# Kernel tuning notes

Measured on AMD Instinct MI355X. Metric: run time of the kernel, lower is better.

## Reference

```python
import jax, jax.numpy as jnp
import numpy as np

A_, H_, D_, T_, B_ = 12, 6, 192, 80, 8
C_ = 192                      # GATv2 out_channels per head
N_ = B_ * A_                  # sequences
G_ = B_ * T_                  # graphs (one per frame)
E_ = A_ * (A_ - 1)            # 132 directed edges, no self loops
DH_ = D_ // H_


def _ln(x, g, b):
    m = jnp.mean(x, -1, keepdims=True)
    v = jnp.mean((x - m) ** 2, -1, keepdims=True)
    return (x - m) * jax.lax.rsqrt(v + 1e-5) * g + b


def _bn(x, g, b, m, v):  # eval-mode BatchNorm1d over the feature channel
    return (x - m) * jax.lax.rsqrt(v + 1e-5) * g + b


def _forward(state_feat, edge_attr, emb_table, laW1, lab1, bn1g, bn1b, bn1m, bn1v, laW2, lab2, bn2g, bn2b, bn2m, bn2v, laW3, lab3, bn3g, bn3b, bn3m, bn3v, ln1g, ln1b, qkvw, qkvb, outw, outb, ln2g, ln2b, fw1, fb1, fw2, fb2, gwl, gbl, gwr, gbr, gwe, gatt, gbias, ng, nb, padding_mask, agent_ids, edge_index):
    pl = emb_table[jnp.clip(agent_ids, 0)]                                   # [N,12]
    x = jnp.concatenate([state_feat, jnp.broadcast_to(pl[:, None, :], (N_, T_, 12))], -1)
    x = jax.nn.relu(_bn(x @ laW1 + lab1, bn1g, bn1b, bn1m, bn1v))
    x = jax.nn.relu(_bn(x @ laW2 + lab2, bn2g, bn2b, bn2m, bn2v))
    x = jax.nn.relu(_bn(x @ laW3 + lab3, bn3g, bn3b, bn3m, bn3v))
    x_initial = x
    # sinusoidal positional encoding (dropout off / eval)
    pos = jnp.arange(T_, dtype=jnp.float32)[:, None]
    div = jnp.exp(jnp.arange(0, D_, 2, dtype=jnp.float32) * (-np.log(10000.0) / D_))
    pe = jnp.zeros((T_, D_), jnp.float32).at[:, 0::2].set(jnp.sin(pos * div)).at[:, 1::2].set(jnp.cos(pos * div))
    x = x + pe
    causal = jnp.triu(jnp.full((T_, T_), -jnp.inf, jnp.float32), k=1)
    # --- static GAT edge structure (shared by every frame-graph) ---
    src, dst = edge_index[0], edge_index[1]
    onehot = (dst[None, :] == jnp.arange(A_)[:, None]).astype(jnp.float32)   # [A,E]
    cnt = onehot.sum(1)
    ea = edge_attr.reshape(G_, E_, 2)
    # PyG add_self_loops(fill_value='mean'): self-loop attr = mean of incoming-edge attrs
    loop_ea = jnp.einsum('ae,gef->gaf', onehot, ea) / cnt[None, :, None]     # [G,A,2]
    ea2 = jnp.concatenate([ea, loop_ea], axis=1).reshape(-1, 2)              # [G*(E+A),2]
    src2 = jnp.concatenate([src, jnp.arange(A_, dtype=src.dtype)])
    dst2 = jnp.concatenate([dst, jnp.arange(A_, dtype=dst.dtype)])
    off = (jnp.arange(G_, dtype=src.dtype) * A_)[:, None]
    sflat = (src2[None, :] + off).reshape(-1)                                # flattened batch-of-graphs
    dflat = (dst2[None, :] + off).reshape(-1)
    GA = G_ * A_
    for l in range(3):
        # --- causal temporal self-attention (pre-LN, eval: dropout off) ---
        xn = _ln(x, ln1g[l], ln1b[l])
        qkv = xn @ qkvw[l] + qkvb[l]
        q, k, v = jnp.split(qkv, 3, axis=-1)
        q = q.reshape(N_, T_, H_, DH_); k = k.reshape(N_, T_, H_, DH_); v = v.reshape(N_, T_, H_, DH_)
        s = jnp.einsum('nqhd,nkhd->nhqk', q, k) / np.sqrt(DH_) + causal
        s = jnp.where(padding_mask[:, None, None, :], -jnp.inf, s)
        p = jax.nn.softmax(s, axis=-1)
        o = jnp.einsum('nhqk,nkhd->nqhd', p, v).reshape(N_, T_, D_)
        x = x + (o @ outw[l] + outb[l])
        xn = _ln(x, ln2g[l], ln2b[l])
        x = x + (jax.nn.gelu(xn @ fw1[l] + fb1[l], approximate=False) @ fw2[l] + fb2[l])
        # --- framewise GATv2 (concat=False -> mean over heads) ---
        xn = _ln(x, ng[l], nb[l])
        xnodes = xn.reshape(B_, A_, T_, D_).transpose(0, 2, 1, 3).reshape(GA, D_)
        xl = (xnodes @ gwl[l] + gbl[l]).reshape(GA, H_, C_)
        xr = (xnodes @ gwr[l] + gbr[l]).reshape(GA, H_, C_)
        ef = (ea2 @ gwe[l]).reshape(-1, H_, C_)
        xls = xl[sflat]                                                      # gather source features
        msg = jax.nn.leaky_relu(xls + xr[dflat] + ef, 0.2)
        alpha = jnp.einsum('ehc,hc->eh', msg, gatt[l])
        amax = jax.lax.stop_gradient(jax.ops.segment_max(alpha, dflat, num_segments=GA))
        exs = jnp.exp(alpha - amax[dflat])
        den = jax.ops.segment_sum(exs, dflat, num_segments=GA)
        w = exs / den[dflat]                                                 # segment softmax over dst
        agg = jax.ops.segment_sum(w[:, :, None] * xls, dflat, num_segments=GA)
        xg = (agg.mean(axis=1) + gbias[l]).reshape(B_, T_, A_, D_).transpose(0, 2, 1, 3).reshape(N_, T_, D_)
        x = x + xg
    return (x_initial, x)


def setup_inputs():
    ks = iter(jax.random.split(jax.random.key(0), 60))
    def r(shape, s=0.05):
        return jax.random.normal(next(ks), shape, jnp.float32) * s
    pairs = np.array([(i, j) for i in range(A_) for j in range(A_) if i != j], dtype=np.int32)
    return dict(
        state_feat=jax.random.normal(next(ks), (N_, T_, 4), jnp.float32),
        padding_mask=jnp.zeros((N_, T_), bool),
        agent_ids=jax.random.randint(next(ks), (N_,), 0, 600, jnp.int32),
        edge_index=jnp.asarray(pairs.T),
        edge_attr=jax.random.normal(next(ks), (B_, T_, E_, 2), jnp.float32),
        emb_table=r((600, 12), 1.0),
        laW1=r((16, 64)), lab1=jnp.zeros((64,)),
        bn1g=jnp.ones((64,)), bn1b=jnp.zeros((64,)), bn1m=jnp.zeros((64,)), bn1v=jnp.ones((64,)),
        laW2=r((64, 256)), lab2=jnp.zeros((256,)),
        bn2g=jnp.ones((256,)), bn2b=jnp.zeros((256,)), bn2m=jnp.zeros((256,)), bn2v=jnp.ones((256,)),
        laW3=r((256, D_)), lab3=jnp.zeros((D_,)),
        bn3g=jnp.ones((D_,)), bn3b=jnp.zeros((D_,)), bn3m=jnp.zeros((D_,)), bn3v=jnp.ones((D_,)),
        ln1g=jnp.ones((3, D_)), ln1b=jnp.zeros((3, D_)),
        qkvw=r((3, D_, 3 * D_)), qkvb=jnp.zeros((3, 3 * D_)),
        outw=r((3, D_, D_)), outb=jnp.zeros((3, D_)),
        ln2g=jnp.ones((3, D_)), ln2b=jnp.zeros((3, D_)),
        fw1=r((3, D_, 4 * D_)), fb1=jnp.zeros((3, 4 * D_)),
        fw2=r((3, 4 * D_, D_)), fb2=jnp.zeros((3, D_)),
        gwl=r((3, D_, H_ * C_)), gbl=jnp.zeros((3, H_ * C_)),
        gwr=r((3, D_, H_ * C_)), gbr=jnp.zeros((3, H_ * C_)),
        gwe=r((3, 2, H_ * C_)),
        gatt=r((3, H_, C_)),
        gbias=jnp.zeros((3, D_)),
        ng=jnp.ones((3, D_)), nb=jnp.zeros((3, D_)),
    )


def reference(state_feat, padding_mask, agent_ids, edge_index, edge_attr, emb_table, laW1, lab1, bn1g, bn1b, bn1m, bn1v, laW2, lab2, bn2g, bn2b, bn2m, bn2v, laW3, lab3, bn3g, bn3b, bn3m, bn3v, ln1g, ln1b, qkvw, qkvb, outw, outb, ln2g, ln2b, fw1, fb1, fw2, fb2, gwl, gbl, gwr, gbr, gwe, gatt, gbias, ng, nb):
    return _forward(state_feat, edge_attr, emb_table, laW1, lab1, bn1g, bn1b, bn1m, bn1v, laW2, lab2, bn2g, bn2b, bn2m, bn2v, laW3, lab3, bn3g, bn3b, bn3m, bn3v, ln1g, ln1b, qkvw, qkvb, outw, outb, ln2g, ln2b, fw1, fb1, fw2, fb2, gwl, gbl, gwr, gbr, gwe, gatt, gbias, ng, nb, padding_mask, agent_ids, edge_index)
```

## Files before the change

### kernel.cpp

```cpp
#include <hip/hip_runtime.h>
#include <hip/hip_bf16.h>
#include <math.h>

#define A_   12
#define H_   6
#define N_   96
#define T_   80
#define G_   640
#define E_   132
#define E2_  144
#define ROWS_ 7680

typedef const __hip_bfloat16* bfp;
typedef __hip_bfloat16 bf16;
typedef __attribute__((ext_vector_type(8))) short short8;
typedef __attribute__((ext_vector_type(4))) short short4v;
typedef __attribute__((ext_vector_type(4))) float f32x4;
typedef _Float16 h2 __attribute__((ext_vector_type(2)));

#define WB_QKV   0
#define WB_OUT   331776
#define WB_FW1   442368
#define WB_FW2   884736
#define WB_GAT   1327104
#define WB_W1    2654208
#define WB_W2    2655232
#define WB_W3T   2671616
#define WB_GWE   2720768
#define WB_GATT  2727680
#define WB_TOT   2731136
#define BB_QKV   0
#define BB_OUT   1728
#define BB_FW1   2304
#define BB_FW2   4608
#define BB_GAT   5184
#define BB_B1    12096
#define BB_B2    12160
#define BB_B3    12416
#define BB_TOT   12608

__device__ __forceinline__ float b2f(bf16 x){ return __bfloat162float(x); }
__device__ __forceinline__ float ldf(const void* p, size_t i, int f){
    return f ? __bfloat162float(((const bf16*)p)[i]) : ((const float*)p)[i];
}

__global__ void k_detect(const void* sf, int* flag)
{
    const unsigned short* u = (const unsigned short*)sf;
    int sane = 0;
    for (int i = 0; i < 64; i++){
        unsigned short v = u[2*i];
        int e = (v >> 7) & 0xFF;
        if (e == 0 || (e >= 100 && e <= 140)) sane++;
    }
    *flag = (sane >= 48) ? 1 : 0;
}

__global__ __launch_bounds__(256) void k_convert(
    const void* qkvw, const void* outw, const void* fw1, const void* fw2,
    const void* gwl, const void* gwr, const void* gwe, const void* gatt,
    const void* W1, const void* b1, const void* g1, const void* be1, const void* m1, const void* v1,
    const void* W2, const void* b2, const void* g2, const void* be2, const void* m2, const void* v2,
    const void* W3, const void* b3, const void* g3, const void* be3, const void* m3, const void* v3,
    const void* qkvb, const void* outb, const void* fb1, const void* fb2,
    const void* gbl, const void* gbr,
    const int* flagp, bf16* WB, float* BB)
{
    const int f = *flagp;
    size_t idx = (size_t)blockIdx.x*256 + threadIdx.x;
    if (idx < WB_TOT){
        float v; int ishalf = 0;
        if (idx < WB_OUT){            size_t i=idx-WB_QKV; int l=i/110592; int r=i%110592; int n=r/192, k=r%192;
            v = ldf(qkvw, (size_t)l*110592 + (size_t)k*576 + n, f);
        } else if (idx < WB_FW1){     size_t i=idx-WB_OUT; int l=i/36864; int r=i%36864; int n=r/192, k=r%192;
            v = ldf(outw, (size_t)l*36864 + (size_t)k*192 + n, f);
        } else if (idx < WB_FW2){     size_t i=idx-WB_FW1; int l=i/147456; int r=i%147456; int n=r/192, k=r%192;
            v = ldf(fw1, (size_t)l*147456 + (size_t)k*768 + n, f);
        } else if (idx < WB_GAT){     size_t i=idx-WB_FW2; int l=i/147456; int r=i%147456; int n=r/768, k=r%768;
            v = ldf(fw2, (size_t)l*147456 + (size_t)k*192 + n, f);
        } else if (idx < WB_W1){      size_t i=idx-WB_GAT; int l=i/442368; int r=i%442368; int n=r/192, k=r%192;
            if (n < 1152) v = ldf(gwl, (size_t)l*221184 + (size_t)k*1152 + n, f);
            else          v = ldf(gwr, (size_t)l*221184 + (size_t)k*1152 + (n-1152), f);
        } else if (idx < WB_W2){      size_t i=idx-WB_W1; int o=i%64;
            float s = ldf(g1,o,f)*rsqrtf(ldf(v1,o,f)+1e-5f);
            v = ldf(W1, i, f) * s;
        } else if (idx < WB_W3T){     size_t i=idx-WB_W2; int o=i%256;
            float s = ldf(g2,o,f)*rsqrtf(ldf(v2,o,f)+1e-5f);
            v = ldf(W2, i, f) * s;
        } else if (idx < WB_GWE){     size_t i=idx-WB_W3T; int n=i/256, k=i%256;
            float s = ldf(g3,n,f)*rsqrtf(ldf(v3,n,f)+1e-5f);
            v = ldf(W3, (size_t)k*192 + n, f) * s;
        } else if (idx < WB_GATT){    size_t i=idx-WB_GWE;
            v = ldf(gwe, i, f); ishalf = 1;
        } else {                      size_t i=idx-WB_GATT;
            v = ldf(gatt, i, f); ishalf = 1;
        }
        if (ishalf) ((_Float16*)WB)[idx] = (_Float16)v;
        else        WB[idx] = __float2bfloat16(v);
    } else if (idx < WB_TOT + BB_TOT){
        size_t j = idx - WB_TOT;
        float v;
        if (j < BB_OUT)        v = ldf(qkvb, j, f);
        else if (j < BB_FW1)   v = ldf(outb, j-BB_OUT, f);
        else if (j < BB_FW2)   v = ldf(fb1, j-BB_FW1, f);
        else if (j < BB_GAT)   v = ldf(fb2, j-BB_FW2, f);
        else if (j < BB_B1){   size_t i=j-BB_GAT; int l=i/2304; int o=i%2304;
            v = (o<1152) ? ldf(gbl, (size_t)l*1152+o, f) : ldf(gbr, (size_t)l*1152+o-1152, f);
        } else if (j < BB_B2){ int o=j-BB_B1;
            float s = ldf(g1,o,f)*rsqrtf(ldf(v1,o,f)+1e-5f);
            v = (ldf(b1,o,f)-ldf(m1,o,f))*s + ldf(be1,o,f);
        } else if (j < BB_B3){ int o=j-BB_B2;
            float s = ldf(g2,o,f)*rsqrtf(ldf(v2,o,f)+1e-5f);
            v = (ldf(b2,o,f)-ldf(m2,o,f))*s + ldf(be2,o,f);
        } else {               int o=j-BB_B3;
            float s = ldf(g3,o,f)*rsqrtf(ldf(v3,o,f)+1e-5f);
            v = (ldf(b3,o,f)-ldf(m3,o,f))*s + ldf(be3,o,f);
        }
        BB[j] = v;
    }
}

__global__ __launch_bounds__(256) void k_mlp_a(
    const void* sf, const int* ids, const void* emb, const int* flagp,
    const bf16* __restrict__ WB, const float* __restrict__ BB, bf16* h2g)
{
    __shared__ float in16[16][16];
    __shared__ float h1[16][64];
    const int f = *flagp;
    int tid = threadIdx.x;
    int row0 = blockIdx.x * 16;
    {
        int r = tid >> 4, i = tid & 15;
        int row = row0 + r;
        float v;
        if (i < 4) v = ldf(sf, (size_t)row*4 + i, f);
        else {
            int id = ids[row / T_]; if (id < 0) id = 0; if (id > 599) id = 599;
            v = ldf(emb, (size_t)id*12 + (i-4), f);
        }
        in16[r][i] = v;
    }
    __syncthreads();
    {
        int o = tid & 63, rg = tid >> 6;
        float acc[4];
        float bv = BB[BB_B1 + o];
        #pragma unroll
        for (int j=0;j<4;j++) acc[j] = bv;
        for (int i=0;i<16;i++){
            float w = b2f(WB[WB_W1 + i*64 + o]);
            #pragma unroll
            for (int j=0;j<4;j++) acc[j] += in16[rg*4+j][i]*w;
        }
        #pragma unroll
        for (int j=0;j<4;j++) h1[rg*4+j][o] = acc[j] > 0.f ? acc[j] : 0.f;
    }
    __syncthreads();
    {
        int o = tid;
        float acc[16];
        float bv = BB[BB_B2 + o];
        #pragma unroll
        for (int r=0;r<16;r++) acc[r] = bv;
        for (int i=0;i<64;i++){
            float w = b2f(WB[WB_W2 + i*256 + o]);
            #pragma unroll
            for (int r=0;r<16;r++) acc[r] += h1[r][i]*w;
        }
        for (int r=0;r<16;r++){
            float v = acc[r] > 0.f ? acc[r] : 0.f;
            h2g[(size_t)(row0+r)*256 + o] = __float2bfloat16(v);
        }
    }
}

__global__ __launch_bounds__(256) void k_mgemm(
    const bf16* __restrict__ A, const bf16* __restrict__ Wt, const float* __restrict__ bias,
    bf16* outh, float* outf, const float* __restrict__ res, void* out0, const int* flagp,
    int K, int N, int mode)
{
    __shared__ short As[64*200];
    __shared__ short Bs[64*200];
    int tid = threadIdx.x;
    int w = tid >> 6, lane = tid & 63, q = lane >> 4, li = lane & 15;
    int m0 = blockIdx.x * 64, n0 = blockIdx.y * 64;
    const int f = flagp ? *flagp : 0;
    f32x4 acc[4];
    #pragma unroll
    for (int nt=0;nt<4;nt++) acc[nt] = (f32x4){0.f,0.f,0.f,0.f};
    int nkc = (K + 191) / 192;
    for (int kc = 0; kc < nkc; kc++){
        int kcw = K - kc*192; if (kcw > 192) kcw = 192;
        int vr = kcw >> 3;
        const bf16* Ab = A  + (size_t)m0*K + kc*192;
        const bf16* Bb = Wt + (size_t)n0*K + kc*192;
        for (int idx = tid; idx < 64*vr; idx += 256){
            int r = idx / vr, kv = idx - r*vr;
            *(short8*)&As[r*200 + kv*8] = *(const short8*)&Ab[(size_t)r*K + kv*8];
        }
        for (int idx = tid; idx < 64*vr; idx += 256){
            int r = idx / vr, kv = idx - r*vr;
            *(short8*)&Bs[r*200 + kv*8] = *(const short8*)&Bb[(size_t)r*K + kv*8];
        }
        __syncthreads();
        int kkn = kcw >> 5;
        for (int kk = 0; kk < kkn; kk++){
            int ko = kk*32 + q*8;
            short8 a = *(short8*)&As[(w*16+li)*200 + ko];
            #pragma unroll
            for (int nt = 0; nt < 4; nt++){
                short8 b = *(short8*)&Bs[(nt*16+li)*200 + ko];
                acc[nt] = __builtin_amdgcn_mfma_f32_16x16x32_bf16(a, b, acc[nt], 0, 0, 0);
            }
        }
        __syncthreads();
    }
    int rb = m0 + w*16 + q*4;
    #pragma unroll
    for (int nt = 0; nt < 4; nt++){
        int col = n0 + nt*16 + li;
        float bv = bias[col];
        #pragma unroll
        for (int p = 0; p < 4; p++){
            int row = rb + p;
            float v = acc[nt][p] + bv;
            size_t idx = (size_t)row*N + col;
            if (mode == 0) outh[idx] = __float2bfloat16(v);
            else if (mode == 1) outh[idx] = __float2bfloat16(0.5f*v*(1.f + erff(v*0.70710678118654752f)));
            else if (mode == 2) outf[idx] = v + res[idx];
            else {
                float r2 = v > 0.f ? v : 0.f;
                if (f) ((bf16*)out0)[idx] = __float2bfloat16(r2);
                else   ((float*)out0)[idx] = r2;
                int t = row % T_;
                int i2 = col & ~1;
                float dv = expf((float)i2 * (-9.210340371976184f/192.f));
                float ang = (float)t * dv;
                outf[idx] = r2 + ((col & 1) ? cosf(ang) : sinf(ang));
            }
        }
    }
}

__global__ __launch_bounds__(256) void k_mgemm128(
    const bf16* __restrict__ A, const bf16* __restrict__ Wt, const float* __restrict__ bias,
    bf16* outh, int K, int N, int mode)
{
    __shared__ short As[128*104];
    __shared__ short Bs[64*104];
    int tid = threadIdx.x;
    int w = tid >> 6, lane = tid & 63, q = lane >> 4, li = lane & 15;
    int m0 = blockIdx.x * 128, n0 = blockIdx.y * 64;
    f32x4 acc[2][4];
    #pragma unroll
    for (int mt=0;mt<2;mt++)
        #pragma unroll
        for (int nt=0;nt<4;nt++) acc[mt][nt] = (f32x4){0.f,0.f,0.f,0.f};
    int nkc = K / 96;
    for (int kc = 0; kc < nkc; kc++){
        const bf16* Ab = A  + (size_t)m0*K + kc*96;
        const bf16* Bb = Wt + (size_t)n0*K + kc*96;
        for (int idx = tid; idx < 128*12; idx += 256){
            int r = idx / 12, kv = idx - r*12;
            *(short8*)&As[r*104 + kv*8] = *(const short8*)&Ab[(size_t)r*K + kv*8];
        }
        for (int idx = tid; idx < 64*12; idx += 256){
            int r = idx / 12, kv = idx - r*12;
            *(short8*)&Bs[r*104 + kv*8] = *(const short8*)&Bb[(size_t)r*K + kv*8];
        }
        __syncthreads();
        #pragma unroll
        for (int kk = 0; kk < 3; kk++){
            int ko = kk*32 + q*8;
            short8 b0 = *(short8*)&Bs[(0*16+li)*104 + ko];
            short8 b1 = *(short8*)&Bs[(1*16+li)*104 + ko];
            short8 b2 = *(short8*)&Bs[(2*16+li)*104 + ko];
            short8 b3 = *(short8*)&Bs[(3*16+li)*104 + ko];
            #pragma unroll
            for (int mt = 0; mt < 2; mt++){
                short8 a = *(short8*)&As[(w*32 + mt*16 + li)*104 + ko];
                acc[mt][0] = __builtin_amdgcn_mfma_f32_16x16x32_bf16(a, b0, acc[mt][0], 0, 0, 0);
                acc[mt][1] = __builtin_amdgcn_mfma_f32_16x16x32_bf16(a, b1, acc[mt][1], 0, 0, 0);
                acc[mt][2] = __builtin_amdgcn_mfma_f32_16x16x32_bf16(a, b2, acc[mt][2], 0, 0, 0);
                acc[mt][3] = __builtin_amdgcn_mfma_f32_16x16x32_bf16(a, b3, acc[mt][3], 0, 0, 0);
            }
        }
        __syncthreads();
    }
    #pragma unroll
    for (int mt = 0; mt < 2; mt++){
        int rb = m0 + w*32 + mt*16 + q*4;
        #pragma unroll
        for (int nt = 0; nt < 4; nt++){
            int col = n0 + nt*16 + li;
            float bv = bias[col];
            #pragma unroll
            for (int p = 0; p < 4; p++){
                float v = acc[mt][nt][p] + bv;
                size_t idx = (size_t)(rb+p)*N + col;
                if (mode == 0) outh[idx] = __float2bfloat16(v);
                else if (mode == 1) outh[idx] = __float2bfloat16(0.5f*v*(1.f + erff(v*0.70710678118654752f)));
                else ((_Float16*)outh)[idx] = (_Float16)v;
            }
        }
    }
}

__global__ __launch_bounds__(256) void k_ln(const float* __restrict__ x, const void* g, const void* b,
                     size_t gOff, const int* flagp, bf16* out, int permute)
{
    const int f = *flagp;
    int tid = threadIdx.x;
    int row = blockIdx.x*4 + (tid>>6);
    int lane = tid & 63;
    const float* xr = x + (size_t)row*192;
    float v0 = xr[lane], v1 = xr[lane+64], v2 = xr[lane+128];
    float s = v0+v1+v2;
    float qq = v0*v0+v1*v1+v2*v2;
    #pragma unroll
    for (int off=32; off; off>>=1){ s += __shfl_xor(s, off); qq += __shfl_xor(qq, off); }
    float mean = s * (1.f/192.f);
    float var  = qq * (1.f/192.f) - mean*mean;
    float rs = rsqrtf(var + 1e-5f);
    int orow = row;
    if (permute){ int n = row/T_, t = row%T_; int bb = n/A_, a = n%A_; orow = (bb*T_+t)*A_ + a; }
    bf16* op = out + (size_t)orow*192;
    op[lane]     = __float2bfloat16((v0-mean)*rs*ldf(g,gOff+lane,f)     + ldf(b,gOff+lane,f));
    op[lane+64]  = __float2bfloat16((v1-mean)*rs*ldf(g,gOff+lane+64,f)  + ldf(b,gOff+lane+64,f));
    op[lane+128] = __float2bfloat16((v2-mean)*rs*ldf(g,gOff+lane+128,f) + ldf(b,gOff+lane+128,f));
}

__global__ __launch_bounds__(64) void k_attn(bfp qkv, bf16* attn_o)
{
    __shared__ float Ks[80][32];
    __shared__ float Vs[80][32];
    int bid = blockIdx.x;
    int qt = bid % 5;
    int nh = bid / 5;
    int n = nh / H_, h = nh % H_;
    int tid = threadIdx.x;
    for (int idx = tid; idx < 640; idx += 64){
        int r = idx >> 3, c4 = (idx & 7) << 2;
        const bf16* rp = qkv + (size_t)(n*T_+r)*576 + h*32 + c4;
        short4v kv = *(const short4v*)(rp + 192);
        short4v vv = *(const short4v*)(rp + 384);
        f32x4 kf, vf;
        #pragma unroll
        for (int e=0;e<4;e++){
            kf[e] = __uint_as_float(((unsigned)(unsigned short)kv[e])<<16);
            vf[e] = __uint_as_float(((unsigned)(unsigned short)vv[e])<<16);
        }
        *(f32x4*)&Ks[r][c4] = kf;
        *(f32x4*)&Vs[r][c4] = vf;
    }
    __syncthreads();
    int qi = tid & 15, p = tid >> 4;
    int q = qt*16 + qi;
    float qv[8];
    const bf16* qp = qkv + (size_t)(n*T_+q)*576 + h*32 + p*8;
    #pragma unroll
    for (int c=0;c<8;c++) qv[c] = b2f(qp[c]);
    float m = -1e30f, l = 0.f;
    float acc[8];
    #pragma unroll
    for (int c=0;c<8;c++) acc[c]=0.f;
    int jmax = qt*16 + 15;
    for (int j = 0; j <= jmax; j++){
        float s = 0.f;
        #pragma unroll
        for (int c=0;c<8;c++) s += qv[c]*Ks[j][p*8+c];
        s += __shfl_xor(s, 16);
        s += __shfl_xor(s, 32);
        s *= 0.17677669529663687f;
        if (j > q) s = -1e30f;
        float mn = fmaxf(m, s);
        float corr = expf(m - mn);
        float e = expf(s - mn);
        l = l*corr + e;
        #pragma unroll
        for (int c=0;c<8;c++) acc[c] = acc[c]*corr + e*Vs[j][p*8+c];
        m = mn;
    }
    float inv = 1.f/l;
    bf16* op = attn_o + (size_t)(n*T_+q)*192 + h*32 + p*8;
    #pragma unroll
    for (int c=0;c<8;c++) op[c] = __float2bfloat16(acc[c]*inv);
}

__global__ __launch_bounds__(192) void k_loopea(const int* __restrict__ eidx, const void* ea,
                                                const int* flagp, float* lea)
{
    __shared__ float s0[A_], s1[A_];
    __shared__ int cnt[A_];
    const int f = *flagp;
    int g = blockIdx.x;
    int tid = threadIdx.x;
    if (tid < A_){ s0[tid] = 0.f; s1[tid] = 0.f; cnt[tid] = 0; }
    __syncthreads();
    if (tid < E_){
        int d = eidx[E_ + tid];
        float a0 = ldf(ea, (size_t)(g*E_+tid)*2,   f);
        float a1 = ldf(ea, (size_t)(g*E_+tid)*2+1, f);
        atomicAdd(&s0[d], a0);
        atomicAdd(&s1[d], a1);
        atomicAdd(&cnt[d], 1);
    }
    __syncthreads();
    if (tid < A_){
        int c = cnt[tid] < 1 ? 1 : cnt[tid];
        lea[(g*A_+tid)*2]   = s0[tid]/(float)c;
        lea[(g*A_+tid)*2+1] = s1[tid]/(float)c;
    }
}

__global__ __launch_bounds__(256) void k_alpha(const _Float16* __restrict__ xlr,
                        const float* __restrict__ lea, const void* ea,
                        const _Float16* __restrict__ gweh, const _Float16* __restrict__ gatth,
                        const int* flagp, float* alpha)
{
    const int f = *flagp;
    int bid = blockIdx.x;
    int xcd = bid & 7, slot = bid >> 3;
    int g = xcd*80 + slot/9;
    int unit = (slot % 9)*4 + (threadIdx.x>>6);
    int d = unit / 3, sg = unit % 3;
    int lane = threadIdx.x & 63;
    int co = 6*lane;
    const h2 c06 = (h2){(_Float16)0.6f, (_Float16)0.6f};
    const h2 c04 = (h2){(_Float16)0.4f, (_Float16)0.4f};
    h2 xr[9], g0[9], g1[9], ga[9];
    const _Float16* xrd = xlr + (size_t)(g*A_+d)*2304 + 1152;
    #pragma unroll
    for (int hg = 0; hg < 3; hg++)
        #pragma unroll
        for (int j = 0; j < 3; j++){
            int o = hg*384 + co + 2*j;
            int i = hg*3 + j;
            xr[i] = *(const h2*)(xrd + o);
            g0[i] = *(const h2*)(gweh + o);
            g1[i] = *(const h2*)(gweh + 1152 + o);
            ga[i] = *(const h2*)(gatth + o);
        }
    for (int si = 0; si < 4; si++){
        int s = sg*4 + si;
        float f0, f1;
        if (s == d){
            f0 = lea[(g*A_+s)*2]; f1 = lea[(g*A_+s)*2+1];
        } else {
            int el = s*11 + (d < s ? d : d-1);
            f0 = ldf(ea, (size_t)(g*E_+el)*2,   f);
            f1 = ldf(ea, (size_t)(g*E_+el)*2+1, f);
        }
        h2 f0h = (h2){(_Float16)f0, (_Float16)f0};
        h2 f1h = (h2){(_Float16)f1, (_Float16)f1};
        const _Float16* xls = xlr + (size_t)(g*A_+s)*2304;
        float* ap = alpha + ((size_t)(g*A_+d)*12 + s)*H_;
        #pragma unroll
        for (int hg = 0; hg < 3; hg++){
            float p = 0.f;
            #pragma unroll
            for (int j = 0; j < 3; j++){
                int o = hg*384 + co + 2*j;
                int i = hg*3 + j;
                h2 xl2 = *(const h2*)(xls + o);
                h2 m = xl2 + xr[i];
                m = g0[i]*f0h + m;
                m = g1[i]*f1h + m;
                unsigned mu = __builtin_bit_cast(unsigned, m) & 0x7fff7fffu;
                h2 am = __builtin_bit_cast(h2, mu);
                h2 q = m*c06 + am*c04;
                p = __builtin_amdgcn_fdot2(ga[i], q, p, false);
            }
            #pragma unroll
            for (int off=1; off<32; off<<=1) p += __shfl_xor(p, off);
            if ((lane & 31) == 0)
                ap[hg*2 + (lane>>5)] = p;
        }
    }
}

__global__ __launch_bounds__(192) void k_segagg(const _Float16* __restrict__ xlr,
                         const float* __restrict__ alpha,
                         const void* gbias, size_t gbOff, const int* flagp, float* xf,
                         void* out)
{
    __shared__ float al[12][6];
    __shared__ float w[12][6];
    const int f = *flagp;
    int bid = blockIdx.x;
    int xcd = bid & 7, slot = bid >> 3;
    int gl = xcd*80 + slot/12;
    int a = slot % 12;
    int node = gl*A_ + a;
    int tid = threadIdx.x;
    if (tid < 72) ((float*)al)[tid] = alpha[(size_t)node*72 + tid];
    __syncthreads();
    if (tid < 6){
        float m = -1e30f;
        #pragma unroll
        for (int s=0;s<12;s++) m = fmaxf(m, al[s][tid]);
        float den = 0.f;
        #pragma unroll
        for (int s=0;s<12;s++){ float ex = expf(al[s][tid]-m); w[s][tid] = ex; den += ex; }
        float inv = 1.f/den;
        #pragma unroll
        for (int s=0;s<12;s++) w[s][tid] *= inv;
    }
    __syncthreads();
    int c = tid;
    float acc = 0.f;
    for (int s=0;s<12;s++){
        const _Float16* xp = xlr + (size_t)(gl*A_ + s)*2304 + c;
        #pragma unroll
        for (int h=0;h<6;h++) acc += w[s][h]*(float)xp[h*192];
    }
    int b = gl / T_, t = gl % T_;
    int xrow = (b*A_ + a)*T_ + t;
    size_t idx = (size_t)xrow*192 + c;
    float newv = xf[idx] + acc*(1.f/6.f) + ldf(gbias, gbOff + c, f);
    xf[idx] = newv;
    if (out){
        if (f) ((bf16*)out)[1474560 + idx] = __float2bfloat16(newv);
        else   ((float*)out)[1474560 + idx] = newv;
    }
}

extern "C" void kernel_launch(void* const* d_in, const int* in_sizes, int n_in,
                              void* d_out, int out_size, void* d_ws, size_t ws_size,
                              hipStream_t stream)
{
    const void* sf   = d_in[0];
    const int* ids  = (const int*)d_in[2];
    const int* eidx = (const int*)d_in[3];
    const void* ea   = d_in[4];
    const void* emb  = d_in[5];
    const void *laW1=d_in[6],  *lab1=d_in[7];
    const void *bn1g=d_in[8],  *bn1b=d_in[9],  *bn1m=d_in[10], *bn1v=d_in[11];
    const void *laW2=d_in[12], *lab2=d_in[13];
    const void *bn2g=d_in[14], *bn2b=d_in[15], *bn2m=d_in[16], *bn2v=d_in[17];
    const void *laW3=d_in[18], *lab3=d_in[19];
    const void *bn3g=d_in[20], *bn3b=d_in[21], *bn3m=d_in[22], *bn3v=d_in[23];
    const void *ln1g=d_in[24], *ln1b=d_in[25];
    const void *qkvw=d_in[26], *qkvb=d_in[27];
    const void *outw=d_in[28], *outb=d_in[29];
    const void *ln2g=d_in[30], *ln2b=d_in[31];
    const void *fw1 =d_in[32], *fb1 =d_in[33];
    const void *fw2 =d_in[34], *fb2 =d_in[35];
    const void *gwl =d_in[36], *gbl =d_in[37];
    const void *gwr =d_in[38], *gbr =d_in[39];
    const void *gwe =d_in[40];
    const void *gatt=d_in[41];
    const void *gbias=d_in[42];
    const void *ng  =d_in[43], *nb  =d_in[44];

    float* ws = (float*)d_ws;
    float* xf  = ws;
    bf16*  xn  = (bf16*)(ws + 1474560);
    bf16*  qkv = (bf16*)(ws + 2211840);
    bf16*  ao  = (bf16*)(ws + 4423680);
    bf16*  hb  = (bf16*)(ws + 2211840);
    bf16*  h2g = (bf16*)(ws + 2211840);
    bf16*  xlr = (bf16*)(ws + 2211840);
    float* lea = ws + 11059200;
    int*  flag = (int*)(ws + 11074560);
    bf16*  WB  = (bf16*)(ws + 11074568);
    float* BB  = ws + 12440136;
    float* alp = ws + 12452744;
    (void)ws_size; (void)in_sizes; (void)n_in; (void)out_size;

    k_detect<<<1, 1, 0, stream>>>(sf, flag);
    k_convert<<<(WB_TOT+BB_TOT+255)/256, 256, 0, stream>>>(
        qkvw, outw, fw1, fw2, gwl, gwr, gwe, gatt,
        laW1, lab1, bn1g, bn1b, bn1m, bn1v,
        laW2, lab2, bn2g, bn2b, bn2m, bn2v,
        laW3, lab3, bn3g, bn3b, bn3m, bn3v,
        qkvb, outb, fb1, fb2, gbl, gbr, flag, WB, BB);
    k_mlp_a<<<ROWS_/16, 256, 0, stream>>>(sf, ids, emb, flag, WB, BB, h2g);
    k_mgemm<<<dim3(ROWS_/64, 3), 256, 0, stream>>>(h2g, WB + WB_W3T, BB + BB_B3,
        nullptr, xf, nullptr, d_out, flag, 256, 192, 3);
    k_loopea<<<G_, 192, 0, stream>>>(eidx, ea, flag, lea);

    for (int l=0; l<3; l++){
        k_ln<<<ROWS_/4, 256, 0, stream>>>(xf, ln1g, ln1b, (size_t)l*192, flag, xn, 0);
        k_mgemm128<<<dim3(ROWS_/128, 9), 256, 0, stream>>>(xn, WB + WB_QKV + (size_t)l*110592,
            BB + BB_QKV + l*576, qkv, 192, 576, 0);
        k_attn<<<N_*H_*5, 64, 0, stream>>>(qkv, ao);
        k_mgemm<<<dim3(ROWS_/64, 3), 256, 0, stream>>>(ao, WB + WB_OUT + (size_t)l*36864,
            BB + BB_OUT + l*192, nullptr, xf, xf, nullptr, nullptr, 192, 192, 2);
        k_ln<<<ROWS_/4, 256, 0, stream>>>(xf, ln2g, ln2b, (size_t)l*192, flag, xn, 0);
        k_mgemm128<<<dim3(ROWS_/128, 12), 256, 0, stream>>>(xn, WB + WB_FW1 + (size_t)l*147456,
            BB + BB_FW1 + l*768, hb, 192, 768, 1);
        k_mgemm<<<dim3(ROWS_/64, 3), 256, 0, stream>>>(hb, WB + WB_FW2 + (size_t)l*147456,
            BB + BB_FW2 + l*192, nullptr, xf, xf, nullptr, nullptr, 768, 192, 2);
        k_ln<<<ROWS_/4, 256, 0, stream>>>(xf, ng, nb, (size_t)l*192, flag, xn, 1);
        k_mgemm128<<<dim3(ROWS_/128, 36), 256, 0, stream>>>(xn, WB + WB_GAT + (size_t)l*442368,
            BB + BB_GAT + l*2304, xlr, 192, 2304, 4);
        k_alpha<<<G_*36/4, 256, 0, stream>>>((const _Float16*)xlr, lea, ea,
            (const _Float16*)(WB + WB_GWE) + (size_t)l*2304,
            (const _Float16*)(WB + WB_GATT) + (size_t)l*1152, flag, alp);
        k_segagg<<<G_*A_, 192, 0, stream>>>((const _Float16*)xlr, alp, gbias, (size_t)l*192, flag, xf,
            l == 2 ? d_out : nullptr);
    }
}
```

Measured before the change: 809.9 us.

## Fuse next-layer LayerNorm into GAT aggregation and merge attention query tiles

k_segagg now also computes the next layer's ln1 LayerNorm over the updated residual row and writes the bf16 normalized output, so the separate k_ln launch is skipped for layers 1 and 2. k_attn now uses one 320-thread block per (sequence, head) covering all five query tiles, instead of five 64-thread blocks. This loads K/V into shared memory once per head instead of five times. The trade-off is fewer, larger attention blocks with uneven causal work across waves, plus a block-wide reduction and an extra __syncthreads in segagg.

```diff
diff --git a/kernel.cpp b/kernel.cpp
--- a/kernel.cpp
+++ b/kernel.cpp
@@ -330,16 +330,14 @@
     op[lane+128] = __float2bfloat16((v2-mean)*rs*ldf(g,gOff+lane+128,f) + ldf(b,gOff+lane+128,f));
 }
 
-__global__ __launch_bounds__(64) void k_attn(bfp qkv, bf16* attn_o)
+__global__ __launch_bounds__(320) void k_attn(bfp qkv, bf16* attn_o)
 {
     __shared__ float Ks[80][32];
     __shared__ float Vs[80][32];
-    int bid = blockIdx.x;
-    int qt = bid % 5;
-    int nh = bid / 5;
+    int nh = blockIdx.x;
     int n = nh / H_, h = nh % H_;
     int tid = threadIdx.x;
-    for (int idx = tid; idx < 640; idx += 64){
+    for (int idx = tid; idx < 640; idx += 320){
         int r = idx >> 3, c4 = (idx & 7) << 2;
         const bf16* rp = qkv + (size_t)(n*T_+r)*576 + h*32 + c4;
         short4v kv = *(const short4v*)(rp + 192);
@@ -354,7 +352,9 @@
         *(f32x4*)&Vs[r][c4] = vf;
     }
     __syncthreads();
-    int qi = tid & 15, p = tid >> 4;
+    int qt = tid >> 6;
+    int lane = tid & 63;
+    int qi = lane & 15, p = lane >> 4;
     int q = qt*16 + qi;
     float qv[8];
     const bf16* qp = qkv + (size_t)(n*T_+q)*576 + h*32 + p*8;
@@ -482,10 +482,11 @@
 __global__ __launch_bounds__(192) void k_segagg(const _Float16* __restrict__ xlr,
                          const float* __restrict__ alpha,
                          const void* gbias, size_t gbOff, const int* flagp, float* xf,
-                         void* out)
+                         void* out, const void* lng, const void* lnb, size_t lnOff, bf16* xn_out)
 {
     __shared__ float al[12][6];
     __shared__ float w[12][6];
+    __shared__ float sred[3], qred[3];
     const int f = *flagp;
     int bid = blockIdx.x;
     int xcd = bid & 7, slot = bid >> 3;
@@ -522,6 +523,20 @@
     if (out){
         if (f) ((bf16*)out)[1474560 + idx] = __float2bfloat16(newv);
         else   ((float*)out)[1474560 + idx] = newv;
+    }
+    if (xn_out){
+        float sv = newv, qv2 = newv*newv;
+        #pragma unroll
+        for (int off=32; off; off>>=1){ sv += __shfl_xor(sv, off); qv2 += __shfl_xor(qv2, off); }
+        int wid = tid >> 6;
+        if ((tid & 63) == 0){ sred[wid] = sv; qred[wid] = qv2; }
+        __syncthreads();
+        float S = sred[0] + sred[1] + sred[2];
+        float Q = qred[0] + qred[1] + qred[2];
+        float mean = S * (1.f/192.f);
+        float var  = Q * (1.f/192.f) - mean*mean;
+        float rs = rsqrtf(var + 1e-5f);
+        xn_out[idx] = __float2bfloat16((newv-mean)*rs*ldf(lng, lnOff+c, f) + ldf(lnb, lnOff+c, f));
     }
 }
 
@@ -581,10 +596,11 @@
     k_loopea<<<G_, 192, 0, stream>>>(eidx, ea, flag, lea);
 
     for (int l=0; l<3; l++){
-        k_ln<<<ROWS_/4, 256, 0, stream>>>(xf, ln1g, ln1b, (size_t)l*192, flag, xn, 0);
+        if (l == 0)
+            k_ln<<<ROWS_/4, 256, 0, stream>>>(xf, ln1g, ln1b, 0, flag, xn, 0);
         k_mgemm128<<<dim3(ROWS_/128, 9), 256, 0, stream>>>(xn, WB + WB_QKV + (size_t)l*110592,
             BB + BB_QKV + l*576, qkv, 192, 576, 0);
-        k_attn<<<N_*H_*5, 64, 0, stream>>>(qkv, ao);
+        k_attn<<<N_*H_, 320, 0, stream>>>(qkv, ao);
         k_mgemm<<<dim3(ROWS_/64, 3), 256, 0, stream>>>(ao, WB + WB_OUT + (size_t)l*36864,
             BB + BB_OUT + l*192, nullptr, xf, xf, nullptr, nullptr, 192, 192, 2);
         k_ln<<<ROWS_/4, 256, 0, stream>>>(xf, ln2g, ln2b, (size_t)l*192, flag, xn, 0);
@@ -599,6 +615,8 @@
             (const _Float16*)(WB + WB_GWE) + (size_t)l*2304,
             (const _Float16*)(WB + WB_GATT) + (size_t)l*1152, flag, alp);
         k_segagg<<<G_*A_, 192, 0, stream>>>((const _Float16*)xlr, alp, gbias, (size_t)l*192, flag, xf,
-            l == 2 ? d_out : nullptr);
-    }
-}
+            l == 2 ? d_out : nullptr,
+            l < 2 ? ln1g : nullptr, ln1b, (size_t)(l+1)*192,
+            l < 2 ? xn : nullptr);
+    }
+}
```

After: 795.7 us. No clear change (-1.7%).
